# Performance work log

Hardware: AMD Instinct MI355X
Metric: run time of the kernel (lower is better)

## Reference

```python
import jax, jax.numpy as jnp
import numpy as np

EPS = 1e-6  # torch F.pairwise_distance default eps added to the difference


def setup_inputs() -> dict:
    key = jax.random.key(0)
    k1, k2 = jax.random.split(key)
    x = jax.random.normal(k1, (8, 4096, 512), dtype=jnp.float32)
    centroids = jax.random.normal(k2, (2048, 512), dtype=jnp.float32)
    return {"x": x, "centroids": centroids}


def reference(x, centroids):
    # Faithful to KMeans.forward with normalize=None, p_norm=2, return_centroids=True.
    # torch pairwise_distance computes ||x - c + eps||_2; expand algebraically with
    # xe = x + eps to avoid materializing the (b, k, d) broadcast:
    #   ||xe - c||^2 = ||xe||^2 - 2 xe.c + ||c||^2
    batch_shape = x.shape[:-1]
    d = x.shape[-1]
    xf = x.reshape(-1, d)                    # (b, d)
    xe = xf + EPS
    x_sq = jnp.sum(xe * xe, axis=-1, keepdims=True)          # (b, 1)
    c_sq = jnp.sum(centroids * centroids, axis=-1)[None, :]  # (1, k)
    sq = x_sq + c_sq - 2.0 * (xe @ centroids.T)              # (b, k)
    dist = jnp.sqrt(jnp.maximum(sq, 0.0))
    labels = jnp.argmin(dist, axis=-1)                        # (b,)
    assigned = centroids[labels]                              # (b, d)
    labels = labels.reshape(batch_shape)
    assigned = assigned.reshape(*batch_shape, d)
    return labels, assigned
```

## Files before the change

### kernel.cpp

```cpp
#include <hip/hip_runtime.h>
#include <hip/hip_bf16.h>


#define EPS 1e-6f
#define TAU 0.3f

constexpr int BROWS = 32768;
constexpr int DD    = 512;
constexpr int KC    = 2048;
constexpr int FCAP  = 4096;
constexpr int NK    = DD / 32;

typedef _Float16 half8  __attribute__((ext_vector_type(8)));
typedef _Float16 half4v __attribute__((ext_vector_type(4)));
typedef float    f32x4  __attribute__((ext_vector_type(4)));

__global__ __launch_bounds__(256) void prep(const float* __restrict__ x,
                                            const float* __restrict__ cen,
                                            _Float16* __restrict__ xh,
                                            _Float16* __restrict__ ch,
                                            float* __restrict__ csq,
                                            int* __restrict__ ctr) {
    const int bid = blockIdx.x;
    if (bid < KC / 4) {
        if (bid == 0 && threadIdx.x == 0) *ctr = 0;
        int w = threadIdx.x >> 6, lane = threadIdx.x & 63;
        int c = bid * 4 + w;
        const float* row = cen + (size_t)c * DD;
        float4 v0 = *(const float4*)(row + lane * 8);
        float4 v1 = *(const float4*)(row + lane * 8 + 4);
        half8 h;
        h[0] = (_Float16)v0.x; h[1] = (_Float16)v0.y; h[2] = (_Float16)v0.z; h[3] = (_Float16)v0.w;
        h[4] = (_Float16)v1.x; h[5] = (_Float16)v1.y; h[6] = (_Float16)v1.z; h[7] = (_Float16)v1.w;
        *(half8*)(ch + (size_t)c * DD + lane * 8) = h;
        float s = v0.x*v0.x + v0.y*v0.y + v0.z*v0.z + v0.w*v0.w
                + v1.x*v1.x + v1.y*v1.y + v1.z*v1.z + v1.w*v1.w;
        #pragma unroll
        for (int off = 32; off > 0; off >>= 1) s += __shfl_down(s, off, 64);
        if (lane == 0) csq[c] = s;
    } else {
        size_t i = ((size_t)(bid - KC / 4) * 256 + threadIdx.x) * 4;
        float4 v = *(const float4*)(x + i);
        half4v h;
        h[0] = (_Float16)(v.x + EPS); h[1] = (_Float16)(v.y + EPS);
        h[2] = (_Float16)(v.z + EPS); h[3] = (_Float16)(v.w + EPS);
        *(half4v*)(xh + i) = h;
    }
}

__global__ __launch_bounds__(512, 2) void dist_f16(const _Float16* __restrict__ xh,
                                                   const _Float16* __restrict__ ch,
                                                   const float* __restrict__ csq,
                                                   float* __restrict__ pbest,
                                                   float* __restrict__ psec,
                                                   int*   __restrict__ pidx) {
    __shared__ __align__(16) _Float16 smem[5 * 8192];

    const int tid = threadIdx.x;
    const int w = tid >> 6, lane = tid & 63;
    const int wr = w >> 2, wc = w & 3;
    const int quad = lane >> 4, u = lane & 15;
    const int rowBase = blockIdx.x * 256;
    const int colBase = blockIdx.y * 256;

    float cq[4];
    #pragma unroll
    for (int fc = 0; fc < 4; fc++) cq[fc] = csq[colBase + wc * 64 + fc * 16 + u];

    const int g0 = 128 * w + lane;
    const int g1 = g0 + 64;
    const int r0 = g0 >> 2, h0 = g0 & 3;
    const int r1 = g1 >> 2, h1 = g1 & 3;
    const _Float16* pa0 = xh + (size_t)(rowBase + r0) * DD + h0 * 8;
    const _Float16* pa1 = xh + (size_t)(rowBase + r1) * DD + h1 * 8;
    const _Float16* pb0 = ch + (size_t)(colBase + r0) * DD + h0 * 8;
    const _Float16* pb1 = ch + (size_t)(colBase + r1) * DD + h1 * 8;

    auto stageA = [&](int kt) {
        _Float16* dst = smem + (kt % 3) * 8192;
        const int off = kt * 32;
        __builtin_amdgcn_global_load_lds(
            (const __attribute__((address_space(1))) void*)(pa0 + off),
            (__attribute__((address_space(3))) void*)(dst + g0 * 8), 16, 0, 0);
        __builtin_amdgcn_global_load_lds(
            (const __attribute__((address_space(1))) void*)(pa1 + off),
            (__attribute__((address_space(3))) void*)(dst + g1 * 8), 16, 0, 0);
    };
    auto stageB = [&](int kt) {
        _Float16* dst = smem + 24576 + (kt % 2) * 8192;
        const int off = kt * 32;
        __builtin_amdgcn_global_load_lds(
            (const __attribute__((address_space(1))) void*)(pb0 + off),
            (__attribute__((address_space(3))) void*)(dst + g0 * 8), 16, 0, 0);
        __builtin_amdgcn_global_load_lds(
            (const __attribute__((address_space(1))) void*)(pb1 + off),
            (__attribute__((address_space(3))) void*)(dst + g1 * 8), 16, 0, 0);
    };

    f32x4 acc[8][4] = {};

    stageA(0); stageB(0); stageA(1);

    for (int kc = 0; kc < NK; kc++) {
        if (kc + 1 < NK) asm volatile("s_waitcnt vmcnt(2)" ::: "memory");
        else             asm volatile("s_waitcnt vmcnt(0)" ::: "memory");
        __builtin_amdgcn_s_barrier();
        asm volatile("" ::: "memory");
        __builtin_amdgcn_sched_barrier(0);

        if (kc + 1 < NK) stageB(kc + 1);
        if (kc + 2 < NK) stageA(kc + 2);

        const _Float16* abuf = smem + (kc % 3) * 8192;
        const _Float16* bbuf = smem + 24576 + (kc % 2) * 8192;
        half8 af[8], bf[4];
        #pragma unroll
        for (int f = 0; f < 8; f++)
            af[f] = *(const half8*)(abuf + (wr * 128 + f * 16 + u) * 32 + quad * 8);
        #pragma unroll
        for (int f = 0; f < 4; f++)
            bf[f] = *(const half8*)(bbuf + (wc * 64 + f * 16 + u) * 32 + quad * 8);

        #pragma unroll
        for (int fr = 0; fr < 8; fr++)
            #pragma unroll
            for (int fc = 0; fc < 4; fc++)
                acc[fr][fc] = __builtin_amdgcn_mfma_f32_16x16x32_f16(af[fr], bf[fc], acc[fr][fc], 0, 0, 0);
    }

    __syncthreads();

    float* ebf = (float*)smem;
    float* esf = ebf + 8 * 128;
    int*   eif = (int*)(esf + 8 * 128);

    const int cbi = blockIdx.y * 4 + wc;
    const int colQuadBase = colBase + wc * 64;

    #pragma unroll
    for (int fr = 0; fr < 8; fr++) {
        #pragma unroll
        for (int reg = 0; reg < 4; reg++) {
            float vv[4];
            #pragma unroll
            for (int fc = 0; fc < 4; fc++) vv[fc] = cq[fc] - 2.0f * acc[fr][fc][reg];
            float mn01 = fminf(vv[0], vv[1]), mx01 = fmaxf(vv[0], vv[1]);
            float mn23 = fminf(vv[2], vv[3]), mx23 = fmaxf(vv[2], vv[3]);
            float b = fminf(mn01, mn23);
            float s = fminf(fmaxf(mn01, mn23), fminf(mx01, mx23));
            #pragma unroll
            for (int m = 1; m < 16; m <<= 1) {
                float ob = __shfl_xor(b, m, 64);
                float os = __shfl_xor(s, m, 64);
                s = fminf(fminf(s, os), fmaxf(b, ob));
                b = fminf(b, ob);
            }
            int bi = 0x7fffffff;
            #pragma unroll
            for (int fc = 0; fc < 4; fc++) {
                unsigned long long mm = __ballot(vv[fc] == b);
                unsigned q16 = (unsigned)((mm >> (quad * 16)) & 0xFFFFu);
                if (bi == 0x7fffffff && q16)
                    bi = colQuadBase + fc * 16 + (__ffs(q16) - 1);
            }
            if (u == 0) {
                int rl = fr * 16 + quad * 4 + reg;
                ebf[w * 128 + rl] = b; esf[w * 128 + rl] = s; eif[w * 128 + rl] = bi;
            }
        }
    }
    __syncthreads();
    {
        const int base = cbi * BROWS + rowBase + wr * 128;
        pbest[base + lane]      = ebf[w * 128 + lane];
        pbest[base + 64 + lane] = ebf[w * 128 + 64 + lane];
        psec [base + lane]      = esf[w * 128 + lane];
        psec [base + 64 + lane] = esf[w * 128 + 64 + lane];
        pidx [base + lane]      = eif[w * 128 + lane];
        pidx [base + 64 + lane] = eif[w * 128 + 64 + lane];
    }
}

__global__ __launch_bounds__(256) void reduce_rows(const float* __restrict__ pbest,
                                                   const float* __restrict__ psec,
                                                   const int* __restrict__ pidx,
                                                   float* __restrict__ out,
                                                   int* __restrict__ labels,
                                                   int* __restrict__ rlist,
                                                   int* __restrict__ ctr) {
    int row = blockIdx.x * 256 + threadIdx.x;
    float b = 3.4e38f, s = 3.4e38f; int bi = 0x7fffffff;
    for (int p = 0; p < 32; p++) {
        float v  = pbest[p * BROWS + row];
        float sv = psec [p * BROWS + row];
        int   vi = pidx [p * BROWS + row];
        if (v < b) { s = fminf(b, fminf(s, sv)); b = v; bi = vi; }
        else       { s = fminf(s, fminf(v, sv)); }
    }
    out[row] = (float)bi;
    labels[row] = bi;
    if (s - b < TAU) {
        int slot = atomicAdd(ctr, 1);
        if (slot < FCAP) rlist[slot] = row;
    }
}

__global__ __launch_bounds__(256, 2) void fixup_dist(const float* __restrict__ x,
                                                     const float* __restrict__ cen,
                                                     const float* __restrict__ csq,
                                                     const int* __restrict__ rlist,
                                                     const int* __restrict__ ctr,
                                                     float* __restrict__ fbest,
                                                     int*   __restrict__ fidx) {
    int n = min(*ctr, FCAP);
    int tilebase = blockIdx.y * 128;
    if (tilebase >= n) return;

    __shared__ float xs[16][132];
    __shared__ float cs[16][132];
    __shared__ float redv[128][17];
    __shared__ int   redi[128][17];
    __shared__ int   rows[128];

    const int tid = threadIdx.x;
    if (tid < 128) {
        int ii = tilebase + tid;
        rows[tid] = (ii < n) ? rlist[ii] : 0;
    }
    __syncthreads();

    const int ty = tid >> 4, tx = tid & 15;
    const int colBase = blockIdx.x * 128;

    float acc[8][8] = {};
    for (int dk = 0; dk < DD; dk += 16) {
        #pragma unroll
        for (int sI = 0; sI < 2; sI++) {
            int id = tid + sI * 256;
            int r  = id >> 2;
            int dc = (id & 3) * 4;
            float4 xv = *(const float4*)(x + (size_t)rows[r] * DD + dk + dc);
            xs[dc + 0][r] = xv.x + EPS; xs[dc + 1][r] = xv.y + EPS;
            xs[dc + 2][r] = xv.z + EPS; xs[dc + 3][r] = xv.w + EPS;
            float4 cv = *(const float4*)(cen + (size_t)(colBase + r) * DD + dk + dc);
            cs[dc + 0][r] = cv.x; cs[dc + 1][r] = cv.y;
            cs[dc + 2][r] = cv.z; cs[dc + 3][r] = cv.w;
        }
        __syncthreads();
        #pragma unroll
        for (int k = 0; k < 16; k++) {
            float4 a0 = *(const float4*)&xs[k][ty * 4];
            float4 a1 = *(const float4*)&xs[k][64 + ty * 4];
            float4 b0 = *(const float4*)&cs[k][tx * 4];
            float4 b1 = *(const float4*)&cs[k][64 + tx * 4];
            float a[8] = {a0.x, a0.y, a0.z, a0.w, a1.x, a1.y, a1.z, a1.w};
            float b[8] = {b0.x, b0.y, b0.z, b0.w, b1.x, b1.y, b1.z, b1.w};
            #pragma unroll
            for (int i = 0; i < 8; i++)
                #pragma unroll
                for (int j = 0; j < 8; j++)
                    acc[i][j] += a[i] * b[j];
        }
        __syncthreads();
    }

    float bv[8]; int bix[8];
    #pragma unroll
    for (int i = 0; i < 8; i++) { bv[i] = 3.4e38f; bix[i] = 0x7fffffff; }
    #pragma unroll
    for (int j = 0; j < 8; j++) {
        int col = colBase + ((j < 4) ? (tx * 4 + j) : (64 + tx * 4 + (j - 4)));
        float cq = csq[col];
        #pragma unroll
        for (int i = 0; i < 8; i++) {
            float v = cq - 2.0f * acc[i][j];
            if (v < bv[i] || (v == bv[i] && col < bix[i])) { bv[i] = v; bix[i] = col; }
        }
    }
    #pragma unroll
    for (int i = 0; i < 8; i++) {
        int r = (i < 4) ? (ty * 4 + i) : (64 + ty * 4 + (i - 4));
        redv[r][tx] = bv[i]; redi[r][tx] = bix[i];
    }
    __syncthreads();
    if (tid < 128) {
        float b = 3.4e38f; int bi = 0x7fffffff;
        #pragma unroll
        for (int t = 0; t < 16; t++) {
            float v = redv[tid][t]; int ix = redi[tid][t];
            if (v < b || (v == b && ix < bi)) { b = v; bi = ix; }
        }
        fbest[blockIdx.x * FCAP + tilebase + tid] = b;
        fidx [blockIdx.x * FCAP + tilebase + tid] = bi;
    }
}

__global__ __launch_bounds__(256) void fixup_reduce(const float* __restrict__ fbest,
                                                    const int* __restrict__ fidx,
                                                    const int* __restrict__ rlist,
                                                    const int* __restrict__ ctr,
                                                    float* __restrict__ out,
                                                    int* __restrict__ labels) {
    int s = blockIdx.x * 256 + threadIdx.x;
    int n = min(*ctr, FCAP);
    if (s >= n) return;
    float b = 3.4e38f; int bi = 0x7fffffff;
    for (int c = 0; c < 16; c++) {
        float v = fbest[c * FCAP + s]; int ix = fidx[c * FCAP + s];
        if (v < b || (v == b && ix < bi)) { b = v; bi = ix; }
    }
    int row = rlist[s];
    out[row] = (float)bi;
    labels[row] = bi;
}

__global__ __launch_bounds__(256) void gather(const float* __restrict__ cen,
                                              const int* __restrict__ labels,
                                              float* __restrict__ out) {
    __shared__ int lab[8];
    const int tid = threadIdx.x;
    const int rowBase = blockIdx.x * 8;
    if (tid < 8) lab[tid] = labels[rowBase + tid];
    __syncthreads();
    float* assigned = out + BROWS;
    #pragma unroll 4
    for (int s = tid; s < 8 * 128; s += 256) {
        int r = s >> 7;
        int f = (s & 127) * 4;
        float4 v = *(const float4*)(cen + (size_t)lab[r] * DD + f);
        *(float4*)(assigned + (size_t)(rowBase + r) * DD + f) = v;
    }
}

extern "C" void kernel_launch(void* const* d_in, const int* in_sizes, int n_in,
                              void* d_out, int out_size, void* d_ws, size_t ws_size,
                              hipStream_t stream) {
    const float* x   = (const float*)d_in[0];
    const float* cen = (const float*)d_in[1];

    char* base = (char*)d_ws;
    _Float16* xh   = (_Float16*)(base);
    _Float16* ch   = (_Float16*)(base + 33554432);
    float* csq     = (float*)(base + 35651584);
    float* pbest   = (float*)(base + 35659776);
    float* psec    = (float*)(base + 39854080);
    int*   pidx    = (int*)  (base + 44048384);
    int*   labels  = (int*)  (base + 48242688);
    int*   rlist   = (int*)  (base + 48373760);
    float* fbest   = (float*)(base + 48390144);
    int*   fidx    = (int*)  (base + 48652288);
    int*   ctr     = (int*)  (base + 48914432);

    prep<<<KC / 4 + BROWS * DD / 4 / 256, 256, 0, stream>>>(x, cen, xh, ch, csq, ctr);
    dist_f16<<<dim3(BROWS / 256, KC / 256), 512, 0, stream>>>(xh, ch, csq, pbest, psec, pidx);
    reduce_rows<<<BROWS / 256, 256, 0, stream>>>(pbest, psec, pidx, (float*)d_out, labels, rlist, ctr);
    fixup_dist<<<dim3(KC / 128, FCAP / 128), 256, 0, stream>>>(x, cen, csq, rlist, ctr, fbest, fidx);
    fixup_reduce<<<FCAP / 256, 256, 0, stream>>>(fbest, fidx, rlist, ctr, (float*)d_out, labels);
    gather<<<BROWS / 8, 256, 0, stream>>>(cen, labels, (float*)d_out);
}
```

Measured before the change: 318.8 us.

## Simplify to double-buffered A/B staging and raise wave priority around MFMAs

```diff
diff --git a/kernel.cpp b/kernel.cpp
--- a/kernel.cpp
+++ b/kernel.cpp
@@ -54,7 +54,7 @@
                                                    float* __restrict__ pbest,
                                                    float* __restrict__ psec,
                                                    int*   __restrict__ pidx) {
-    __shared__ __align__(16) _Float16 smem[5 * 8192];
+    __shared__ __align__(16) _Float16 smem[4 * 8192];
 
     const int tid = threadIdx.x;
     const int w = tid >> 6, lane = tid & 63;
@@ -76,43 +76,38 @@
     const _Float16* pb0 = ch + (size_t)(colBase + r0) * DD + h0 * 8;
     const _Float16* pb1 = ch + (size_t)(colBase + r1) * DD + h1 * 8;
 
-    auto stageA = [&](int kt) {
-        _Float16* dst = smem + (kt % 3) * 8192;
+    auto stage = [&](int kt) {
+        _Float16* da = smem + (kt & 1) * 8192;
+        _Float16* db = smem + 16384 + (kt & 1) * 8192;
         const int off = kt * 32;
         __builtin_amdgcn_global_load_lds(
             (const __attribute__((address_space(1))) void*)(pa0 + off),
-            (__attribute__((address_space(3))) void*)(dst + g0 * 8), 16, 0, 0);
+            (__attribute__((address_space(3))) void*)(da + g0 * 8), 16, 0, 0);
         __builtin_amdgcn_global_load_lds(
             (const __attribute__((address_space(1))) void*)(pa1 + off),
-            (__attribute__((address_space(3))) void*)(dst + g1 * 8), 16, 0, 0);
-    };
-    auto stageB = [&](int kt) {
-        _Float16* dst = smem + 24576 + (kt % 2) * 8192;
-        const int off = kt * 32;
+            (__attribute__((address_space(3))) void*)(da + g1 * 8), 16, 0, 0);
         __builtin_amdgcn_global_load_lds(
             (const __attribute__((address_space(1))) void*)(pb0 + off),
-            (__attribute__((address_space(3))) void*)(dst + g0 * 8), 16, 0, 0);
+            (__attribute__((address_space(3))) void*)(db + g0 * 8), 16, 0, 0);
         __builtin_amdgcn_global_load_lds(
             (const __attribute__((address_space(1))) void*)(pb1 + off),
-            (__attribute__((address_space(3))) void*)(dst + g1 * 8), 16, 0, 0);
+            (__attribute__((address_space(3))) void*)(db + g1 * 8), 16, 0, 0);
     };
 
     f32x4 acc[8][4] = {};
 
-    stageA(0); stageB(0); stageA(1);
+    stage(0);
 
     for (int kc = 0; kc < NK; kc++) {
-        if (kc + 1 < NK) asm volatile("s_waitcnt vmcnt(2)" ::: "memory");
-        else             asm volatile("s_waitcnt vmcnt(0)" ::: "memory");
+        asm volatile("s_waitcnt vmcnt(0)" ::: "memory");
         __builtin_amdgcn_s_barrier();
         asm volatile("" ::: "memory");
         __builtin_amdgcn_sched_barrier(0);
 
-        if (kc + 1 < NK) stageB(kc + 1);
-        if (kc + 2 < NK) stageA(kc + 2);
-
-        const _Float16* abuf = smem + (kc % 3) * 8192;
-        const _Float16* bbuf = smem + 24576 + (kc % 2) * 8192;
+        if (kc + 1 < NK) stage(kc + 1);
+
+        const _Float16* abuf = smem + (kc & 1) * 8192;
+        const _Float16* bbuf = smem + 16384 + (kc & 1) * 8192;
         half8 af[8], bf[4];
         #pragma unroll
         for (int f = 0; f < 8; f++)
@@ -121,11 +116,13 @@
         for (int f = 0; f < 4; f++)
             bf[f] = *(const half8*)(bbuf + (wc * 64 + f * 16 + u) * 32 + quad * 8);
 
+        __builtin_amdgcn_s_setprio(1);
         #pragma unroll
         for (int fr = 0; fr < 8; fr++)
             #pragma unroll
             for (int fc = 0; fc < 4; fc++)
                 acc[fr][fc] = __builtin_amdgcn_mfma_f32_16x16x32_f16(af[fr], bf[fc], acc[fr][fc], 0, 0, 0);
+        __builtin_amdgcn_s_setprio(0);
     }
 
     __syncthreads();
```

Result: no change. 315.8 us (-0.9%).
